# Optimization experiments

Measured on AMD Instinct MI355X. Metric: run time of the kernel, lower is better.

## Reference

```python
import jax, jax.numpy as jnp
import numpy as np

HIDDEN = 512
HEADS = 8
HEAD_DIM = HIDDEN // HEADS  # 64
NUM_FEATURES = 256
EPS = 1e-4


def _gaussian_orthogonal_random_matrix(num_rows, num_cols, scaling=0, seed=1234):
    """Blocks of orthogonal rows from QR of gaussian matrices, rescaled (FAVOR+)."""
    rng = np.random.default_rng(seed)
    blocks = []
    full_blocks = num_rows // num_cols
    for _ in range(full_blocks):
        q, _ = np.linalg.qr(rng.standard_normal((num_cols, num_cols)))
        blocks.append(q.T)
    rem = num_rows - full_blocks * num_cols
    if rem > 0:
        q, _ = np.linalg.qr(rng.standard_normal((num_cols, num_cols)))
        blocks.append(q.T[:rem])
    mat = np.concatenate(blocks, axis=0)  # [num_rows, num_cols]
    if scaling == 0:
        # row norms of a fresh gaussian matrix (chi-distributed multipliers)
        multiplier = np.linalg.norm(rng.standard_normal((num_rows, num_cols)), axis=1)
    else:
        multiplier = np.sqrt(num_cols) * np.ones(num_rows)
    return (multiplier[:, None] * mat).astype(np.float32)


def _split_heads(x, b):
    # [b, n, hidden] -> [b, h, n, head_dim]
    return x.reshape(b, -1, HEADS, HEAD_DIM).transpose(0, 2, 1, 3)


def _phi(data, proj):
    """Nonnegative softmax kernel feature map (FAVOR+).
    data: [b,h,n,d], proj: [m,d] -> [b,h,n,m]"""
    d = data.shape[-1]
    m = proj.shape[0]
    x = data * (d ** -0.25)
    dash = jnp.einsum('bhnd,md->bhnm', x, proj)
    diag = 0.5 * jnp.sum(x * x, axis=-1, keepdims=True)
    return (m ** -0.5) * jnp.exp(dash - diag) + EPS


def setup_inputs() -> dict:
    key = jax.random.key(0)
    ks = jax.random.split(key, 12)
    b, n = 2, 8192
    s = HIDDEN ** -0.5
    inp = {
        'query': jax.random.normal(ks[0], (b, n, HIDDEN), jnp.float32),
        'key':   jax.random.normal(ks[1], (b, n, HIDDEN), jnp.float32),
        'value': jax.random.normal(ks[2], (b, n, HIDDEN), jnp.float32),
        'WQ_w': jax.random.normal(ks[3], (HIDDEN, HIDDEN), jnp.float32) * s,
        'WQ_b': jnp.zeros((HIDDEN,), jnp.float32),
        'WK_w': jax.random.normal(ks[4], (HIDDEN, HIDDEN), jnp.float32) * s,
        'WK_b': jnp.zeros((HIDDEN,), jnp.float32),
        'WV_w': jax.random.normal(ks[5], (HIDDEN, HIDDEN), jnp.float32) * s,
        'WV_b': jnp.zeros((HIDDEN,), jnp.float32),
        'WO_w': jax.random.normal(ks[6], (HIDDEN, HIDDEN), jnp.float32) * s,
        'WO_b': jnp.zeros((HIDDEN,), jnp.float32),
        'proj': jnp.asarray(_gaussian_orthogonal_random_matrix(NUM_FEATURES, HEAD_DIM)),
    }
    return inp


def reference(query, key, value, WQ_w, WQ_b, WK_w, WK_b, WV_w, WV_b, WO_w, WO_b, proj):
    b = query.shape[0]
    # torch Linear: y = x @ W.T + b
    Q = _split_heads(jnp.einsum('bnd,ed->bne', query, WQ_w) + WQ_b, b)
    K = _split_heads(jnp.einsum('bnd,ed->bne', key,   WK_w) + WK_b, b)
    V = _split_heads(jnp.einsum('bnd,ed->bne', value, WV_w) + WV_b, b)

    Qp = _phi(Q, proj)  # [b,h,n,m]
    Kp = _phi(K, proj)  # [b,h,n,m]

    # denominator: Q' @ sum_n K'  -> [b,h,n,1]
    denom = jnp.einsum('bhnm,bhm->bhn', Qp, jnp.sum(Kp, axis=2))[..., None]
    # linear attention: Q' @ (K'^T V), O(n*m*d)
    ctx = jnp.einsum('bhnm,bhnd->bhmd', Kp, V)
    attn = jnp.einsum('bhnm,bhmd->bhnd', Qp, ctx) / denom

    # faithful to original: .view(batch, -1, hidden) directly on [b,h,n,d]
    attn = attn.reshape(b, -1, HIDDEN)
    return jnp.einsum('bnd,ed->bne', attn, WO_w) + WO_b
```

## Files before the change

kernel.cpp:

```cpp
#include <hip/hip_runtime.h>

typedef __attribute__((ext_vector_type(8))) _Float16 f16x8;
typedef __attribute__((ext_vector_type(4))) float f32x4;

#define S4 0.35355339059327373f

static __device__ __forceinline__ ushort f2h(float f) {
  return __builtin_bit_cast(ushort, (_Float16)f);
}

static __device__ __forceinline__ void gload16(const void* g, void* l) {
  __builtin_amdgcn_global_load_lds((const __attribute__((address_space(1))) void*)g,
                                   (__attribute__((address_space(3))) void*)l, 16, 0, 0);
}

static __device__ __forceinline__ void cvt_store8(ushort* dst, float4 a, float4 b) {
  f16x8 h;
  h[0] = (_Float16)a.x; h[1] = (_Float16)a.y; h[2] = (_Float16)a.z; h[3] = (_Float16)a.w;
  h[4] = (_Float16)b.x; h[5] = (_Float16)b.y; h[6] = (_Float16)b.z; h[7] = (_Float16)b.w;
  *(f16x8*)dst = h;
}

template<int BM, int BN, int WR, int WC, int EPI, int ZMODE, int BF32>
__global__ __launch_bounds__(256) void gemm_bt(
    const ushort* __restrict__ Ah, const void* __restrict__ Bv,
    const float* __restrict__ bias, ushort* __restrict__ Cb,
    float* __restrict__ Cf, const float* __restrict__ rv0,
    int K, int ldA, int ldB, int ldC, int Mz,
    long sAz, long sBz, long sCz)
{
  constexpr int BK = 32;
  constexpr int WTM = BM / WR, WTN = BN / WC;
  constexpr int MI = WTM / 16, NI = WTN / 16;
  constexpr int LDSB = (BM + BN) * 64;

  __shared__ uint4 smem4[LDSB / 16];
  char* smem = (char*)smem4;
  ushort* As = (ushort*)smem;
  ushort* Bs = (ushort*)(smem + BM * 64);

  const int tid = threadIdx.x;
  const int l = tid & 63, w = tid >> 6;
  const int wr = w / WC, wc = w % WC;
  const int lr = l & 15, lk = l >> 4;
  const int tm = blockIdx.x * BM, tn = blockIdx.y * BN;
  const int z = blockIdx.z;

  const ushort* Bh = (const ushort*)Bv;
  const float*  Bf = (const float*)Bv;
  long aoff = 0, boff = 0;
  if (ZMODE == 0) { aoff = (long)z * sAz; boff = (long)z * sBz; }
  if (ZMODE == 2) { aoff = (long)z * sAz; boff = (long)(z >> 3) * sBz + (z & 7) * 64; }
  if (ZMODE == 3) {
    aoff = (long)(z & 15) * sAz + (long)(z >> 4) * 1024;
    boff = (long)(z & 15) * sBz + (long)(z >> 4) * 1024;
  }
  Ah += aoff; Bh += boff; Bf += boff;
  const float* rv = (EPI == 6) ? (rv0 + (long)z * Mz) : nullptr;
  const long coff = (long)z * sCz;

  const int br = tid >> 1, bc = (tid & 1) * 16;
  const float* gB = BF32 ? (Bf + (long)(tn + br) * ldB + bc) : nullptr;
  float4 g0, g1, g2, g3;
  if (BF32) {
    g0 = *(const float4*)(gB);
    g1 = *(const float4*)(gB + 4);
    g2 = *(const float4*)(gB + 8);
    g3 = *(const float4*)(gB + 12);
  }

  f32x4 acc[MI][NI];
#pragma unroll
  for (int i = 0; i < MI; ++i)
#pragma unroll
    for (int j = 0; j < NI; ++j) acc[i][j] = f32x4{0.f, 0.f, 0.f, 0.f};

  for (int k0 = 0; k0 < K; k0 += BK) {
    constexpr int AB = BM * 64;
#pragma unroll
    for (int s = 0; s < (AB + 4095) / 4096; ++s) {
      const int base = s * 4096 + w * 1024;
      if (base < AB) {
        const int idx = base + l * 16;
        gload16(Ah + (long)(tm + (idx >> 6)) * ldA + k0 + ((idx & 63) >> 1),
                (char*)As + base);
      }
    }
    if constexpr (BF32) {
      cvt_store8(Bs + br * 32 + bc, g0, g1);
      cvt_store8(Bs + br * 32 + bc + 8, g2, g3);
    } else {
      constexpr int BB = BN * 64;
#pragma unroll
      for (int s = 0; s < (BB + 4095) / 4096; ++s) {
        const int base = s * 4096 + w * 1024;
        if (base < BB) {
          const int idx = base + l * 16;
          gload16(Bh + (long)(tn + (idx >> 6)) * ldB + k0 + ((idx & 63) >> 1),
                  (char*)Bs + base);
        }
      }
    }
    __syncthreads();

    if (BF32 && k0 + BK < K) {
      const float* gn = gB + k0 + BK;
      g0 = *(const float4*)(gn);
      g1 = *(const float4*)(gn + 4);
      g2 = *(const float4*)(gn + 8);
      g3 = *(const float4*)(gn + 12);
    }

    f16x8 af[MI], bfr[NI];
#pragma unroll
    for (int mi = 0; mi < MI; ++mi)
      af[mi] = *(const f16x8*)(As + (wr * WTM + mi * 16 + lr) * 32 + lk * 8);
#pragma unroll
    for (int ni = 0; ni < NI; ++ni)
      bfr[ni] = *(const f16x8*)(Bs + (wc * WTN + ni * 16 + lr) * 32 + lk * 8);
#pragma unroll
    for (int mi = 0; mi < MI; ++mi)
#pragma unroll
      for (int ni = 0; ni < NI; ++ni)
        acc[mi][ni] = __builtin_amdgcn_mfma_f32_16x16x32_f16(af[mi], bfr[ni], acc[mi][ni], 0, 0, 0);
    __syncthreads();
  }

#pragma unroll
  for (int mi = 0; mi < MI; ++mi) {
#pragma unroll
    for (int j = 0; j < 4; ++j) {
      const int row = tm + wr * WTM + mi * 16 + lk * 4 + j;
#pragma unroll
      for (int ni = 0; ni < NI; ++ni) {
        const int col = tn + wc * WTN + ni * 16 + lr;
        float v = acc[mi][ni][j];
        if (EPI == 3) v += bias[col];
        if (EPI == 4) v += bias[row];
        if (EPI == 6) v = 0.0625f * __expf(v - rv[col]) + 1e-4f;
        if (EPI == 4) {
          const int b = col >> 13, nn = col & 8191;
          const int h = row >> 6, d = row & 63;
          Cb[(long)(b * 8 + h) * 655360 + (long)d * 8192 + nn] = f2h(v);
        } else if (EPI == 3 || EPI == 5) {
          Cf[coff + (long)row * ldC + col] = v;
        } else {
          Cb[coff + (long)row * ldC + col] = f2h(v);
        }
      }
    }
  }
}

__global__ __launch_bounds__(256) void qkproj_k(
    const float* __restrict__ qf, const float* __restrict__ kf,
    const ushort* __restrict__ wqh, const ushort* __restrict__ wkh,
    const float* __restrict__ bq, const float* __restrict__ bk,
    ushort* __restrict__ Qh, ushort* __restrict__ Kh,
    float* __restrict__ diagQ, float* __restrict__ diagK)
{
  const int z = blockIdx.z, qk = z & 1;
  const float*  Af   = qk ? kf : qf;
  const ushort* Bh   = qk ? wkh : wqh;
  const float*  bias = qk ? bk : bq;
  ushort*       Cb   = qk ? Kh : Qh;
  float*        dg   = qk ? diagK : diagQ;
  const int tm = blockIdx.x * 128;
  const int tn = (z >> 1) * 128;

  __shared__ uint4 smem4[1024];
  char* smem = (char*)smem4;
  ushort* As = (ushort*)smem;
  ushort* Bs = (ushort*)(smem + 8192);

  const int tid = threadIdx.x;
  const int l = tid & 63, w = tid >> 6;
  const int wr = w >> 1, wc = w & 1;
  const int lr = l & 15, lk = l >> 4;

  const int ar = tid >> 1, ac = (tid & 1) * 16;
  const float* gA = Af + (long)(tm + ar) * 512 + ac;
  float4 g0 = *(const float4*)(gA);
  float4 g1 = *(const float4*)(gA + 4);
  float4 g2 = *(const float4*)(gA + 8);
  float4 g3 = *(const float4*)(gA + 12);

  f32x4 acc[4][4];
#pragma unroll
  for (int i = 0; i < 4; ++i)
#pragma unroll
    for (int j = 0; j < 4; ++j) acc[i][j] = f32x4{0.f, 0.f, 0.f, 0.f};

  for (int k0 = 0; k0 < 512; k0 += 32) {
    cvt_store8(As + ar * 32 + ac, g0, g1);
    cvt_store8(As + ar * 32 + ac + 8, g2, g3);
#pragma unroll
    for (int s = 0; s < 2; ++s) {
      const int base = s * 4096 + w * 1024;
      const int idx = base + l * 16;
      gload16(Bh + (long)(tn + (idx >> 6)) * 512 + k0 + ((idx & 63) >> 1),
              (char*)Bs + base);
    }
    __syncthreads();

    if (k0 + 32 < 512) {
      const float* gn = gA + k0 + 32;
      g0 = *(const float4*)(gn);
      g1 = *(const float4*)(gn + 4);
      g2 = *(const float4*)(gn + 8);
      g3 = *(const float4*)(gn + 12);
    }

    f16x8 af[4], bfr[4];
#pragma unroll
    for (int mi = 0; mi < 4; ++mi)
      af[mi] = *(const f16x8*)(As + (wr * 64 + mi * 16 + lr) * 32 + lk * 8);
#pragma unroll
    for (int ni = 0; ni < 4; ++ni)
      bfr[ni] = *(const f16x8*)(Bs + (wc * 64 + ni * 16 + lr) * 32 + lk * 8);
#pragma unroll
    for (int mi = 0; mi < 4; ++mi)
#pragma unroll
      for (int ni = 0; ni < 4; ++ni)
        acc[mi][ni] = __builtin_amdgcn_mfma_f32_16x16x32_f16(af[mi], bfr[ni], acc[mi][ni], 0, 0, 0);
    __syncthreads();
  }

#pragma unroll
  for (int mi = 0; mi < 4; ++mi) {
#pragma unroll
    for (int j = 0; j < 4; ++j) {
      const int row = tm + wr * 64 + mi * 16 + lk * 4 + j;
      float ds = 0.f;
#pragma unroll
      for (int ni = 0; ni < 4; ++ni) {
        const int col = tn + wc * 64 + ni * 16 + lr;
        float v = acc[mi][ni][j] + bias[col];
        ds += v * v;
        Cb[(long)row * 512 + col] = f2h(v);
      }
      ds += __shfl_xor(ds, 1, 64);
      ds += __shfl_xor(ds, 2, 64);
      ds += __shfl_xor(ds, 4, 64);
      ds += __shfl_xor(ds, 8, 64);
      if (lr == 0) {
        const int b = row >> 13, nn = row & 8191;
        const int head = (tn + wc * 64) >> 6;
        dg[(long)(b * 8 + head) * 8192 + nn] = 0.0625f * ds;
      }
    }
  }
}

__global__ __launch_bounds__(256) void phiattn_k(
    const ushort* __restrict__ Qh, const ushort* __restrict__ pjh,
    const float* __restrict__ diagQ, const ushort* __restrict__ ctxb,
    ushort* __restrict__ attnR)
{
  const int bx = blockIdx.x, bh = blockIdx.y;
  const int b = bh >> 3, h = bh & 7;
  const int tm = bx * 64;
  const int tid = threadIdx.x, l = tid & 63, w = tid >> 6;
  const int lr = l & 15, lk = l >> 4;

  __shared__ uint4 smem4[4992];
  char* smem = (char*)smem4;
  ushort* P  = (ushort*)smem;
  ushort* Pj = (ushort*)(smem + 33792);
  ushort* As = (ushort*)(smem + 70656);
  ushort* Cs = (ushort*)(smem + 33792);

  const ushort* QB = Qh + (long)b * 4194304 + h * 64;
  const float* rv = diagQ + (long)bh * 8192;

#pragma unroll
  for (int it = 0; it < 8; ++it) {
    const int g = it * 256 + tid;
    const int row = g >> 3, colg = (g & 7) * 8;
    *(uint4*)(Pj + row * 72 + colg) = *(const uint4*)(pjh + row * 64 + colg);
  }
#pragma unroll
  for (int it = 0; it < 2; ++it) {
    const int g = it * 256 + tid;
    const int row = g >> 3, colg = (g & 7) * 8;
    *(uint4*)(As + row * 72 + colg) = *(const uint4*)(QB + (long)(tm + row) * 512 + colg);
  }
  __syncthreads();

  f32x4 a2[16];
#pragma unroll
  for (int i = 0; i < 16; ++i) a2[i] = f32x4{0.f, 0.f, 0.f, 0.f};
  {
    f16x8 af0 = *(const f16x8*)(As + (w * 16 + lr) * 72 + lk * 8);
    f16x8 af1 = *(const f16x8*)(As + (w * 16 + lr) * 72 + 32 + lk * 8);
#pragma unroll
    for (int ni = 0; ni < 16; ++ni) {
      f16x8 b0 = *(const f16x8*)(Pj + (ni * 16 + lr) * 72 + lk * 8);
      f16x8 b1 = *(const f16x8*)(Pj + (ni * 16 + lr) * 72 + 32 + lk * 8);
      a2[ni] = __builtin_amdgcn_mfma_f32_16x16x32_f16(af0, b0, a2[ni], 0, 0, 0);
      a2[ni] = __builtin_amdgcn_mfma_f32_16x16x32_f16(af1, b1, a2[ni], 0, 0, 0);
    }
  }
#pragma unroll
  for (int ni = 0; ni < 16; ++ni)
#pragma unroll
    for (int j = 0; j < 4; ++j) {
      const int row = w * 16 + lk * 4 + j;
      const int col = ni * 16 + lr;
      const float vv = 0.0625f * __expf(a2[ni][j] - rv[tm + row]) + 1e-4f;
      P[row * 264 + col] = f2h(vv);
    }
  __syncthreads();

#pragma unroll
  for (int it = 0; it < 10; ++it) {
    const int g = it * 256 + tid;
    const int row = g >> 5, colg = (g & 31) * 8;
    *(uint4*)(Cs + row * 264 + colg) =
        *(const uint4*)(ctxb + (long)bh * 20480 + row * 256 + colg);
  }
  __syncthreads();

  f32x4 acc[5];
#pragma unroll
  for (int i = 0; i < 5; ++i) acc[i] = f32x4{0.f, 0.f, 0.f, 0.f};

  for (int k0 = 0; k0 < 256; k0 += 32) {
    f16x8 pa = *(const f16x8*)(P + (w * 16 + lr) * 264 + k0 + lk * 8);
#pragma unroll
    for (int ni = 0; ni < 5; ++ni) {
      f16x8 cf = *(const f16x8*)(Cs + (ni * 16 + lr) * 264 + k0 + lk * 8);
      acc[ni] = __builtin_amdgcn_mfma_f32_16x16x32_f16(pa, cf, acc[ni], 0, 0, 0);
    }
  }

  ushort* outb = attnR + (long)bh * 524288;
#pragma unroll
  for (int j = 0; j < 4; ++j) {
    const float dv = __shfl(acc[4][j], (l & 48), 64);
    const int row = tm + w * 16 + lk * 4 + j;
#pragma unroll
    for (int ni = 0; ni < 4; ++ni) {
      const int col = ni * 16 + lr;
      outb[(long)row * 64 + col] = f2h(acc[ni][j] / dv);
    }
  }
}

__global__ __launch_bounds__(256) void cvtall_k(
    const float* __restrict__ wq, const float* __restrict__ wk,
    const float* __restrict__ wv, const float* __restrict__ wo,
    const float* __restrict__ pj,
    ushort* __restrict__ wqh, ushort* __restrict__ wkh,
    ushort* __restrict__ wvh, ushort* __restrict__ woh,
    ushort* __restrict__ pjh, ushort* __restrict__ Vt)
{
  int i = blockIdx.x * 256 + threadIdx.x;
  if (i >= 266240) {
    const int j = i - 266240;
    if (j >= 262144) return;
    const int bh = j >> 14, rem = j & 16383, r = rem >> 10, n8 = rem & 1023;
    const unsigned val = (r == 0) ? 0x3C003C00u : 0u;
    uint4 u; u.x = val; u.y = val; u.z = val; u.w = val;
    *(uint4*)(Vt + (long)bh * 655360 + (long)(64 + r) * 8192 + n8 * 8) = u;
    return;
  }
  const float* in; ushort* out; float scale = 1.f; int idx;
  if (i < 65536)       { in = wq; out = wqh; idx = i; }
  else if (i < 131072) { in = wk; out = wkh; idx = i - 65536; }
  else if (i < 196608) { in = wv; out = wvh; idx = i - 131072; }
  else if (i < 262144) { in = wo; out = woh; idx = i - 196608; }
  else                 { in = pj; out = pjh; idx = i - 262144; scale = S4; }
  float4 f = ((const float4*)in)[idx];
  ushort4 o;
  o.x = f2h(f.x * scale); o.y = f2h(f.y * scale);
  o.z = f2h(f.z * scale); o.w = f2h(f.w * scale);
  ((ushort4*)out)[idx] = o;
}

__global__ __launch_bounds__(256) void ctxred_k(const float* __restrict__ cp,
                                                ushort* __restrict__ ctxb) {
  const int idx = blockIdx.x * 256 + threadIdx.x;
  const int bh = idx / 20480, rem = idx % 20480;
  float a = 0.f;
#pragma unroll
  for (int kc = 0; kc < 8; ++kc) a += cp[(long)(kc * 16 + bh) * 20480 + rem];
  ctxb[idx] = f2h(a);
}

extern "C" void kernel_launch(void* const* d_in, const int* in_sizes, int n_in,
                              void* d_out, int out_size, void* d_ws, size_t ws_size,
                              hipStream_t stream) {
  (void)in_sizes; (void)n_in; (void)out_size; (void)ws_size;
  const float* q  = (const float*)d_in[0];
  const float* k  = (const float*)d_in[1];
  const float* v  = (const float*)d_in[2];
  const float* wq = (const float*)d_in[3];
  const float* bq = (const float*)d_in[4];
  const float* wk = (const float*)d_in[5];
  const float* bk = (const float*)d_in[6];
  const float* wv = (const float*)d_in[7];
  const float* bv = (const float*)d_in[8];
  const float* wo = (const float*)d_in[9];
  const float* bo = (const float*)d_in[10];
  const float* pj = (const float*)d_in[11];

  char* ws = (char*)d_ws;
  ushort* attnR = (ushort*)(ws + 0);
  float*  cpart = (float*)(ws + 16777216);
  ushort* wqh   = (ushort*)(ws + 27262976);
  ushort* wkh   = (ushort*)(ws + 27787264);
  ushort* wvh   = (ushort*)(ws + 28311552);
  ushort* woh   = (ushort*)(ws + 28835840);
  ushort* pjh   = (ushort*)(ws + 29360128);
  ushort* Qh    = (ushort*)(ws + 29392896);
  ushort* Kh    = (ushort*)(ws + 46170112);
  ushort* Vt    = (ushort*)(ws + 62947328);
  ushort* KpT   = (ushort*)(ws + 83918848);
  float*  diagQ = (float*)(ws + 151027712);
  float*  diagK = (float*)(ws + 151552000);
  ushort* ctxb  = (ushort*)(ws + 152076288);

  cvtall_k<<<2064, 256, 0, stream>>>(wq, wk, wv, wo, pj, wqh, wkh, wvh, woh, pjh, Vt);

  qkproj_k<<<dim3(128,1,8), 256, 0, stream>>>(q, k, wqh, wkh, bq, bk,
                                              Qh, Kh, diagQ, diagK);

  gemm_bt<128,128,2,2,4,0,1><<<dim3(4,128,1), 256, 0, stream>>>(
      wvh, v, bv, Vt, nullptr, nullptr, 512, 512, 512, 0, 0, 0L, 0L, 0L);

  gemm_bt<128,128,2,2,6,2,0><<<dim3(2,64,16), 256, 0, stream>>>(
      pjh, Kh, nullptr, KpT, nullptr, diagK, 64, 64, 512, 8192, 8192,
      0L, 4194304L, 2097152L);

  gemm_bt<80,64,1,4,5,3,0><<<dim3(1,4,128), 256, 0, stream>>>(
      Vt, KpT, nullptr, nullptr, cpart, nullptr, 1024, 8192, 8192, 256, 0,
      655360L, 2097152L, 20480L);
  ctxred_k<<<1280, 256, 0, stream>>>(cpart, ctxb);

  phiattn_k<<<dim3(128,16), 256, 0, stream>>>(Qh, pjh, diagQ, ctxb, attnR);

  gemm_bt<128,128,2,2,3,0,0><<<dim3(128,4,1), 256, 0, stream>>>(
      attnR, woh, bo, nullptr, (float*)d_out, nullptr, 512, 512, 512, 512, 0,
      0L, 0L, 0L);
}
```

Measured before the change: 182.1 us.

## Load fp32 operands directly to LDS with XOR swizzle, convert at fragment read

Replaces the register-staged fp32 loads (global load, convert to fp16, store to LDS, with a prefetch for the next k-step) with direct global-to-LDS 16-byte loads of raw fp32 into a row-wise XOR-swizzled layout. The fp32-to-fp16 conversion moves to the point where MFMA fragments are read from LDS. This removes VGPR staging and the explicit LDS store, and the swizzle is meant to avoid bank conflicts. In exchange LDS footprint doubles for the fp32 operand, the cross-iteration register prefetch overlap is lost, and each fp32 element is converted by several waves instead of once.

```diff
diff --git a/kernel.cpp b/kernel.cpp
--- a/kernel.cpp
+++ b/kernel.cpp
@@ -14,11 +14,11 @@
                                    (__attribute__((address_space(3))) void*)l, 16, 0, 0);
 }
 
-static __device__ __forceinline__ void cvt_store8(ushort* dst, float4 a, float4 b) {
+static __device__ __forceinline__ f16x8 cvt8(float4 a, float4 b) {
   f16x8 h;
   h[0] = (_Float16)a.x; h[1] = (_Float16)a.y; h[2] = (_Float16)a.z; h[3] = (_Float16)a.w;
   h[4] = (_Float16)b.x; h[5] = (_Float16)b.y; h[6] = (_Float16)b.z; h[7] = (_Float16)b.w;
-  *(f16x8*)dst = h;
+  return h;
 }
 
 template<int BM, int BN, int WR, int WC, int EPI, int ZMODE, int BF32>
@@ -32,12 +32,12 @@
   constexpr int BK = 32;
   constexpr int WTM = BM / WR, WTN = BN / WC;
   constexpr int MI = WTM / 16, NI = WTN / 16;
-  constexpr int LDSB = (BM + BN) * 64;
+  constexpr int LDSB = BM * 64 + BN * (BF32 ? 128 : 64);
 
   __shared__ uint4 smem4[LDSB / 16];
   char* smem = (char*)smem4;
   ushort* As = (ushort*)smem;
-  ushort* Bs = (ushort*)(smem + BM * 64);
+  char*  Bb  = smem + BM * 64;
 
   const int tid = threadIdx.x;
   const int l = tid & 63, w = tid >> 6;
@@ -59,16 +59,6 @@
   const float* rv = (EPI == 6) ? (rv0 + (long)z * Mz) : nullptr;
   const long coff = (long)z * sCz;
 
-  const int br = tid >> 1, bc = (tid & 1) * 16;
-  const float* gB = BF32 ? (Bf + (long)(tn + br) * ldB + bc) : nullptr;
-  float4 g0, g1, g2, g3;
-  if (BF32) {
-    g0 = *(const float4*)(gB);
-    g1 = *(const float4*)(gB + 4);
-    g2 = *(const float4*)(gB + 8);
-    g3 = *(const float4*)(gB + 12);
-  }
-
   f32x4 acc[MI][NI];
 #pragma unroll
   for (int i = 0; i < MI; ++i)
@@ -87,8 +77,15 @@
       }
     }
     if constexpr (BF32) {
-      cvt_store8(Bs + br * 32 + bc, g0, g1);
-      cvt_store8(Bs + br * 32 + bc + 8, g2, g3);
+      constexpr int BB = BN * 128;
+#pragma unroll
+      for (int s = 0; s < BB / 4096; ++s) {
+        const int base = s * 4096 + w * 1024;
+        const int D = base + l * 16;
+        const int m = D >> 7, slot = (D >> 4) & 7;
+        const int g = slot ^ (m & 7);
+        gload16(Bf + (long)(tn + m) * ldB + k0 + g * 4, Bb + base);
+      }
     } else {
       constexpr int BB = BN * 64;
 #pragma unroll
@@ -97,27 +94,28 @@
         if (base < BB) {
           const int idx = base + l * 16;
           gload16(Bh + (long)(tn + (idx >> 6)) * ldB + k0 + ((idx & 63) >> 1),
-                  (char*)Bs + base);
+                  (char*)Bb + base);
         }
       }
     }
     __syncthreads();
-
-    if (BF32 && k0 + BK < K) {
-      const float* gn = gB + k0 + BK;
-      g0 = *(const float4*)(gn);
-      g1 = *(const float4*)(gn + 4);
-      g2 = *(const float4*)(gn + 8);
-      g3 = *(const float4*)(gn + 12);
-    }
 
     f16x8 af[MI], bfr[NI];
 #pragma unroll
     for (int mi = 0; mi < MI; ++mi)
       af[mi] = *(const f16x8*)(As + (wr * WTM + mi * 16 + lr) * 32 + lk * 8);
 #pragma unroll
-    for (int ni = 0; ni < NI; ++ni)
-      bfr[ni] = *(const f16x8*)(Bs + (wc * WTN + ni * 16 + lr) * 32 + lk * 8);
+    for (int ni = 0; ni < NI; ++ni) {
+      const int row = wc * WTN + ni * 16 + lr;
+      if constexpr (BF32) {
+        const char* rb = Bb + row * 128;
+        float4 f0 = *(const float4*)(rb + ((((lk << 1) | 0) ^ (row & 7)) << 4));
+        float4 f1 = *(const float4*)(rb + ((((lk << 1) | 1) ^ (row & 7)) << 4));
+        bfr[ni] = cvt8(f0, f1);
+      } else {
+        bfr[ni] = *(const f16x8*)((ushort*)Bb + row * 32 + lk * 8);
+      }
+    }
 #pragma unroll
     for (int mi = 0; mi < MI; ++mi)
 #pragma unroll
@@ -168,23 +166,16 @@
   const int tm = blockIdx.x * 128;
   const int tn = (z >> 1) * 128;
 
-  __shared__ uint4 smem4[1024];
+  __shared__ uint4 smem4[1536];
   char* smem = (char*)smem4;
-  ushort* As = (ushort*)smem;
-  ushort* Bs = (ushort*)(smem + 8192);
+  char*   AsF = smem;
+  ushort* Bs  = (ushort*)(smem + 16384);
 
   const int tid = threadIdx.x;
   const int l = tid & 63, w = tid >> 6;
   const int wr = w >> 1, wc = w & 1;
   const int lr = l & 15, lk = l >> 4;
 
-  const int ar = tid >> 1, ac = (tid & 1) * 16;
-  const float* gA = Af + (long)(tm + ar) * 512 + ac;
-  float4 g0 = *(const float4*)(gA);
-  float4 g1 = *(const float4*)(gA + 4);
-  float4 g2 = *(const float4*)(gA + 8);
-  float4 g3 = *(const float4*)(gA + 12);
-
   f32x4 acc[4][4];
 #pragma unroll
   for (int i = 0; i < 4; ++i)
@@ -192,8 +183,14 @@
     for (int j = 0; j < 4; ++j) acc[i][j] = f32x4{0.f, 0.f, 0.f, 0.f};
 
   for (int k0 = 0; k0 < 512; k0 += 32) {
-    cvt_store8(As + ar * 32 + ac, g0, g1);
-    cvt_store8(As + ar * 32 + ac + 8, g2, g3);
+#pragma unroll
+    for (int s = 0; s < 4; ++s) {
+      const int base = s * 4096 + w * 1024;
+      const int D = base + l * 16;
+      const int m = D >> 7, slot = (D >> 4) & 7;
+      const int g = slot ^ (m & 7);
+      gload16(Af + (long)(tm + m) * 512 + k0 + g * 4, AsF + base);
+    }
 #pragma unroll
     for (int s = 0; s < 2; ++s) {
       const int base = s * 4096 + w * 1024;
@@ -203,18 +200,15 @@
     }
     __syncthreads();
 
-    if (k0 + 32 < 512) {
-      const float* gn = gA + k0 + 32;
-      g0 = *(const float4*)(gn);
-      g1 = *(const float4*)(gn + 4);
-      g2 = *(const float4*)(gn + 8);
-      g3 = *(const float4*)(gn + 12);
-    }
-
     f16x8 af[4], bfr[4];
 #pragma unroll
-    for (int mi = 0; mi < 4; ++mi)
-      af[mi] = *(const f16x8*)(As + (wr * 64 + mi * 16 + lr) * 32 + lk * 8);
+    for (int mi = 0; mi < 4; ++mi) {
+      const int row = wr * 64 + mi * 16 + lr;
+      const char* rb = AsF + row * 128;
+      float4 f0 = *(const float4*)(rb + ((((lk << 1) | 0) ^ (row & 7)) << 4));
+      float4 f1 = *(const float4*)(rb + ((((lk << 1) | 1) ^ (row & 7)) << 4));
+      af[mi] = cvt8(f0, f1);
+    }
 #pragma unroll
     for (int ni = 0; ni < 4; ++ni)
       bfr[ni] = *(const f16x8*)(Bs + (wc * 64 + ni * 16 + lr) * 32 + lk * 8);
```

After: 174.8 us. 4.0% less time.
